# Performance work log

Hardware: AMD Instinct MI355X
Metric: run time of the kernel (lower is better)

Reference implementation:

```python
import jax, jax.numpy as jnp
import numpy as np

NEG_BIG = -9e15
ALPHA = 0.2  # LeakyReLU negative slope


def setup_inputs() -> dict:
    key = jax.random.key(0)
    k1, k2, k3, k4 = jax.random.split(key, 4)
    B, N, IN, OUT = 8, 2048, 128, 64
    x = jax.random.normal(k1, (B, N, IN), dtype=jnp.float32)
    adj = jax.random.randint(k2, (B, N, N), 0, 2, dtype=jnp.int32)
    # xavier_uniform with gain=1.414
    lim_W = 1.414 * np.sqrt(6.0 / (IN + OUT))
    W = jax.random.uniform(k3, (IN, OUT), jnp.float32, -lim_W, lim_W)
    lim_a = 1.414 * np.sqrt(6.0 / (2 * OUT + 1))
    a = jax.random.uniform(k4, (2 * OUT, 1), jnp.float32, -lim_a, lim_a)
    return {"x": x, "adj": adj, "W": W, "a": a}


def reference(x, adj, W, a):
    # h: [B, N, out_dim]
    h = jnp.matmul(x, W)
    out_dim = W.shape[1]
    a1 = a[:out_dim, 0]   # applied to h_i (row / destination)
    a2 = a[out_dim:, 0]   # applied to h_j (col / source)
    # e_ij = leakyrelu(h_i . a1 + h_j . a2)  -- avoids the O(B*N*N*2d) concat
    si = jnp.einsum('bnd,d->bn', h, a1)  # [B, N]
    sj = jnp.einsum('bnd,d->bn', h, a2)  # [B, N]
    e = si[:, :, None] + sj[:, None, :]  # [B, N, N]
    e = jnp.where(e > 0, e, ALPHA * e)   # LeakyReLU
    e = jnp.where(adj > 0, e, NEG_BIG)
    attention = jax.nn.softmax(e, axis=-1)  # [B, N, N]
    # dropout p=0.0 (eval mode): identity
    h_prime = jnp.matmul(attention, h)       # [B, N, out_dim]
    return h_prime, attention
```

## Files before the change

### kernel.cpp

```cpp
#include <hip/hip_runtime.h>

#define BB 8
#define NN 2048
#define IND 128
#define OUTD 64
#define ALPHA 0.2f

typedef __attribute__((ext_vector_type(8))) short bf16x8;
typedef __attribute__((ext_vector_type(4))) float f32x4;
typedef unsigned int u32;

__global__ __launch_bounds__(256) void k1_hproj(const float* __restrict__ x,
                                                const float* __restrict__ W,
                                                const float* __restrict__ a,
                                                short* __restrict__ hT_hi,
                                                short* __restrict__ hT_lo,
                                                float* __restrict__ si,
                                                float* __restrict__ sj) {
    __shared__ float Wl[IND * OUTD];
    __shared__ float xl[16][IND];
    __shared__ float tile[16][OUTD + 1];
    int t = threadIdx.x, lane = t & 63, wave = t >> 6;

    const float4* W4 = (const float4*)W;
    float4* Wl4 = (float4*)Wl;
    #pragma unroll
    for (int q = 0; q < 8; ++q) Wl4[t + q * 256] = W4[t + q * 256];

    int row0 = blockIdx.x * 16;
    const float4* x4 = (const float4*)(x + (size_t)row0 * IND);
    float4* xl4 = (float4*)&xl[0][0];
    xl4[t] = x4[t];
    xl4[t + 256] = x4[t + 256];
    __syncthreads();

    float a1v = a[lane];
    float a2v = a[OUTD + lane];

    float acc[4] = {0.f, 0.f, 0.f, 0.f};
    int rbase = wave * 4;
    for (int k = 0; k < IND; k += 4) {
        float4 xv0 = *(const float4*)&xl[rbase + 0][k];
        float4 xv1 = *(const float4*)&xl[rbase + 1][k];
        float4 xv2 = *(const float4*)&xl[rbase + 2][k];
        float4 xv3 = *(const float4*)&xl[rbase + 3][k];
        #pragma unroll
        for (int q = 0; q < 4; ++q) {
            float w = Wl[(k + q) * OUTD + lane];
            acc[0] = fmaf(((const float*)&xv0)[q], w, acc[0]);
            acc[1] = fmaf(((const float*)&xv1)[q], w, acc[1]);
            acc[2] = fmaf(((const float*)&xv2)[q], w, acc[2]);
            acc[3] = fmaf(((const float*)&xv3)[q], w, acc[3]);
        }
    }
    #pragma unroll
    for (int rr = 0; rr < 4; ++rr) {
        size_t grow = (size_t)row0 + rbase + rr;
        tile[rbase + rr][lane] = acc[rr];
        float v1 = acc[rr] * a1v;
        float v2 = acc[rr] * a2v;
        #pragma unroll
        for (int o = 32; o; o >>= 1) {
            v1 += __shfl_xor(v1, o);
            v2 += __shfl_xor(v2, o);
        }
        if (lane == 0) { si[grow] = v1; sj[grow] = v2; }
    }
    __syncthreads();

    int d = t >> 2, kq = (t & 3) * 4;
    int b = row0 >> 11;
    int krow = (row0 & (NN - 1)) + kq;
    float v0 = tile[kq + 0][d], v1 = tile[kq + 1][d];
    float v2 = tile[kq + 2][d], v3 = tile[kq + 3][d];
    u32 b0 = __float_as_uint(v0), b1 = __float_as_uint(v1);
    u32 b2 = __float_as_uint(v2), b3 = __float_as_uint(v3);
    u32 h0 = b0 & 0xffff0000u, h1 = b1 & 0xffff0000u;
    u32 h2 = b2 & 0xffff0000u, h3 = b3 & 0xffff0000u;
    float l0 = v0 - __uint_as_float(h0), l1 = v1 - __uint_as_float(h1);
    float l2 = v2 - __uint_as_float(h2), l3 = v3 - __uint_as_float(h3);
    uint2 hi2, lo2;
    hi2.x = (b0 >> 16) | h1;
    hi2.y = (b2 >> 16) | h3;
    lo2.x = (__float_as_uint(l0) >> 16) | (__float_as_uint(l1) & 0xffff0000u);
    lo2.y = (__float_as_uint(l2) >> 16) | (__float_as_uint(l3) & 0xffff0000u);
    size_t off = ((size_t)b * OUTD + d) * NN + krow;
    *(uint2*)(hT_hi + off) = hi2;
    *(uint2*)(hT_lo + off) = lo2;
}

__global__ __launch_bounds__(512) void k23(const int* __restrict__ adj,
                                           const float* __restrict__ si,
                                           const float* __restrict__ sj,
                                           const short* __restrict__ hT_hi,
                                           const short* __restrict__ hT_lo,
                                           float* __restrict__ attn,
                                           float* __restrict__ hp) {
    __shared__ unsigned char mask_lds[16][264];
    __shared__ float si_lds[16], inv_lds[16];
    __shared__ f32x4 red[8][4][64];

    int t = threadIdx.x, lane = t & 63, w = t >> 6;
    int bk = blockIdx.x;
    int b = bk >> 7;
    int i0 = (bk & 127) * 16;
    size_t rowbase = (size_t)b * NN + i0;
    const float* sjb = sj + (size_t)b * NN;
    const f32x4* sjb4 = (const f32x4*)sjb;

    #pragma unroll
    for (int rr = 0; rr < 2; ++rr) {
        int row = w * 2 + rr;
        size_t grow = rowbase + row;
        float s_i = si[grow];
        const int4* arow = (const int4*)(adj + grow * NN);
        float sum = 0.f;
        #pragma unroll
        for (int q = 0; q < 8; ++q) {
            int4 av = arow[q * 64 + lane];
            f32x4 sv = sjb4[q * 64 + lane];
            unsigned nib = 0;
            float e, pe;
            e = s_i + sv.x; e = e > 0.f ? e : ALPHA * e; pe = __expf(e);
            if (av.x > 0) { nib |= 1u; sum += pe; }
            e = s_i + sv.y; e = e > 0.f ? e : ALPHA * e; pe = __expf(e);
            if (av.y > 0) { nib |= 2u; sum += pe; }
            e = s_i + sv.z; e = e > 0.f ? e : ALPHA * e; pe = __expf(e);
            if (av.z > 0) { nib |= 4u; sum += pe; }
            e = s_i + sv.w; e = e > 0.f ? e : ALPHA * e; pe = __expf(e);
            if (av.w > 0) { nib |= 8u; sum += pe; }
            unsigned pn = (unsigned)__shfl_xor((int)nib, 1);
            if (!(lane & 1))
                mask_lds[row][q * 32 + (lane >> 1)] = (unsigned char)(nib | (pn << 4));
        }
        #pragma unroll
        for (int o = 32; o; o >>= 1) sum += __shfl_xor(sum, o);
        if (lane == 0) {
            si_lds[row] = s_i;
            inv_lds[row] = sum > 0.f ? 1.0f / sum : 0.f;
        }
    }
    __syncthreads();

    {
        f32x4 sv = sjb4[t];
        int mbyte = t >> 1;
        int nshift = (t & 1) * 4;
        #pragma unroll 4
        for (int row = 0; row < 16; ++row) {
            unsigned nib = ((unsigned)mask_lds[row][mbyte] >> nshift) & 0xFu;
            float s_i = si_lds[row], inv = inv_lds[row];
            f32x4 pv;
            float e;
            e = s_i + sv.x; e = e > 0.f ? e : ALPHA * e;
            pv.x = (nib & 1u) ? __expf(e) * inv : 0.f;
            e = s_i + sv.y; e = e > 0.f ? e : ALPHA * e;
            pv.y = (nib & 2u) ? __expf(e) * inv : 0.f;
            e = s_i + sv.z; e = e > 0.f ? e : ALPHA * e;
            pv.z = (nib & 4u) ? __expf(e) * inv : 0.f;
            e = s_i + sv.w; e = e > 0.f ? e : ALPHA * e;
            pv.w = (nib & 8u) ? __expf(e) * inv : 0.f;
            __builtin_nontemporal_store(pv,
                (f32x4*)(attn + (rowbase + row) * (size_t)NN + (size_t)t * 4));
        }
    }

    int m = lane & 15, g = lane >> 4;
    float si_m = si_lds[m];
    float inv_m = inv_lds[m];
    const short* bh_base = hT_hi + ((size_t)b * OUTD + m) * NN;
    const short* bl_base = hT_lo + ((size_t)b * OUTD + m) * NN;

    f32x4 acc[4];
    #pragma unroll
    for (int tt = 0; tt < 4; ++tt) acc[tt] = (f32x4){0.f, 0.f, 0.f, 0.f};

    for (int step = 0; step < 8; ++step) {
        int jb = w * 256 + step * 32 + g * 8;
        f32x4 s0 = *(const f32x4*)(sjb + jb);
        f32x4 s1 = *(const f32x4*)(sjb + jb + 4);
        unsigned mb = mask_lds[m][jb >> 3];
        float sv[8] = {s0.x, s0.y, s0.z, s0.w, s1.x, s1.y, s1.z, s1.w};
        float p[8];
        #pragma unroll
        for (int q = 0; q < 8; ++q) {
            float e = si_m + sv[q];
            e = e > 0.f ? e : ALPHA * e;
            float pe = __expf(e) * inv_m;
            p[q] = ((mb >> q) & 1u) ? pe : 0.f;
        }

        union { bf16x8 v; u32 u[4]; } ph, pl;
        #pragma unroll
        for (int q = 0; q < 4; ++q) {
            u32 c0 = __float_as_uint(p[2 * q]), c1 = __float_as_uint(p[2 * q + 1]);
            u32 t0 = c0 & 0xffff0000u, t1 = c1 & 0xffff0000u;
            float d0 = p[2 * q] - __uint_as_float(t0);
            float d1 = p[2 * q + 1] - __uint_as_float(t1);
            ph.u[q] = (c0 >> 16) | t1;
            pl.u[q] = (__float_as_uint(d0) >> 16) | (__float_as_uint(d1) & 0xffff0000u);
        }

        #pragma unroll
        for (int tt = 0; tt < 4; ++tt) {
            bf16x8 bh = *(const bf16x8*)(bh_base + (size_t)tt * 16 * NN + jb);
            bf16x8 bl = *(const bf16x8*)(bl_base + (size_t)tt * 16 * NN + jb);
            acc[tt] = __builtin_amdgcn_mfma_f32_16x16x32_bf16(ph.v, bh, acc[tt], 0, 0, 0);
            acc[tt] = __builtin_amdgcn_mfma_f32_16x16x32_bf16(ph.v, bl, acc[tt], 0, 0, 0);
            acc[tt] = __builtin_amdgcn_mfma_f32_16x16x32_bf16(pl.v, bh, acc[tt], 0, 0, 0);
        }
    }

    #pragma unroll
    for (int tt = 0; tt < 4; ++tt) red[w][tt][lane] = acc[tt];
    __syncthreads();

    #pragma unroll
    for (int idx = t; idx < 16 * OUTD; idx += 512) {
        int row = idx >> 6, n = idx & 63;
        int ln = (row >> 2) * 16 + (n & 15);
        int reg = row & 3;
        float v = 0.f;
        #pragma unroll
        for (int ww = 0; ww < 8; ++ww)
            v += ((const float*)&red[ww][n >> 4][ln])[reg];
        hp[(rowbase + row) * OUTD + n] = v;
    }
}

extern "C" void kernel_launch(void* const* d_in, const int* in_sizes, int n_in,
                              void* d_out, int out_size, void* d_ws, size_t ws_size,
                              hipStream_t stream) {
    const float* x   = (const float*)d_in[0];
    const int*   adj = (const int*)d_in[1];
    const float* W   = (const float*)d_in[2];
    const float* a   = (const float*)d_in[3];

    float* out  = (float*)d_out;
    float* hp   = out;
    float* attn = out + (size_t)BB * NN * OUTD;

    char* ws = (char*)d_ws;
    short* hT_hi = (short*)ws;
    short* hT_lo = hT_hi + (size_t)BB * OUTD * NN;
    float* si    = (float*)(hT_lo + (size_t)BB * OUTD * NN);
    float* sj    = si + (size_t)BB * NN;

    k1_hproj<<<BB * NN / 16, 256, 0, stream>>>(x, W, a, hT_hi, hT_lo, si, sj);
    k23<<<BB * NN / 16, 512, 0, stream>>>(adj, si, sj, hT_hi, hT_lo, attn, hp);
}
```

Before: 124.9 us.

## Persistent two-tile blocks with register-prefetched adjacency and fused attn/P staging

The k23 kernel becomes persistent: 512 blocks each process two 16-row tiles, and the adjacency rows for the second tile are prefetched into registers while the first tile computes. The separate attention-write pass and the per-wave MFMA probability recompute are merged into one chunked loop. Each wave computes its rows' probabilities once, stores them to attn, and writes bf16 hi/lo splits to LDS, where all waves read them for the MFMA. The goal is to hide adjacency load latency and avoid computing the exponentials twice. In exchange it adds two LDS barriers per chunk, uses heavy register pressure (areg holds 64 VGPRs), and relies on a hand-written lgkmcnt-only barrier.

```diff
diff --git a/kernel.cpp b/kernel.cpp
--- a/kernel.cpp
+++ b/kernel.cpp
@@ -5,10 +5,15 @@
 #define IND 128
 #define OUTD 64
 #define ALPHA 0.2f
+#define NBLK 512
 
 typedef __attribute__((ext_vector_type(8))) short bf16x8;
 typedef __attribute__((ext_vector_type(4))) float f32x4;
 typedef unsigned int u32;
+
+__device__ __forceinline__ void bar_lds() {
+    asm volatile("s_waitcnt lgkmcnt(0)\n\ts_barrier" ::: "memory");
+}
 
 __global__ __launch_bounds__(256) void k1_hproj(const float* __restrict__ x,
                                                 const float* __restrict__ W,
@@ -89,142 +94,158 @@
     *(uint2*)(hT_lo + off) = lo2;
 }
 
-__global__ __launch_bounds__(512) void k23(const int* __restrict__ adj,
-                                           const float* __restrict__ si,
-                                           const float* __restrict__ sj,
-                                           const short* __restrict__ hT_hi,
-                                           const short* __restrict__ hT_lo,
-                                           float* __restrict__ attn,
-                                           float* __restrict__ hp) {
-    __shared__ unsigned char mask_lds[16][264];
-    __shared__ float si_lds[16], inv_lds[16];
+__global__ __launch_bounds__(512, 2) void k23(const int* __restrict__ adj,
+                                              const float* __restrict__ si,
+                                              const float* __restrict__ sj,
+                                              const short* __restrict__ hT_hi,
+                                              const short* __restrict__ hT_lo,
+                                              float* __restrict__ attn,
+                                              float* __restrict__ hp) {
+    __shared__ short p_hi[16][264];
+    __shared__ short p_lo[16][264];
     __shared__ f32x4 red[8][4][64];
 
     int t = threadIdx.x, lane = t & 63, w = t >> 6;
     int bk = blockIdx.x;
-    int b = bk >> 7;
-    int i0 = (bk & 127) * 16;
-    size_t rowbase = (size_t)b * NN + i0;
-    const float* sjb = sj + (size_t)b * NN;
-    const f32x4* sjb4 = (const f32x4*)sjb;
-
-    #pragma unroll
-    for (int rr = 0; rr < 2; ++rr) {
-        int row = w * 2 + rr;
-        size_t grow = rowbase + row;
-        float s_i = si[grow];
-        const int4* arow = (const int4*)(adj + grow * NN);
-        float sum = 0.f;
+    int r0 = w * 2;
+    int m = lane & 15, g = lane >> 4;
+
+    int4 areg[2][8];
+
+    {
+        size_t grow = (size_t)(bk >> 7) * NN + (size_t)(bk & 127) * 16 + r0;
+        const int4* a0 = (const int4*)(adj + grow * NN);
+        const int4* a1 = (const int4*)(adj + (grow + 1) * NN);
         #pragma unroll
         for (int q = 0; q < 8; ++q) {
-            int4 av = arow[q * 64 + lane];
-            f32x4 sv = sjb4[q * 64 + lane];
-            unsigned nib = 0;
-            float e, pe;
-            e = s_i + sv.x; e = e > 0.f ? e : ALPHA * e; pe = __expf(e);
-            if (av.x > 0) { nib |= 1u; sum += pe; }
-            e = s_i + sv.y; e = e > 0.f ? e : ALPHA * e; pe = __expf(e);
-            if (av.y > 0) { nib |= 2u; sum += pe; }
-            e = s_i + sv.z; e = e > 0.f ? e : ALPHA * e; pe = __expf(e);
-            if (av.z > 0) { nib |= 4u; sum += pe; }
-            e = s_i + sv.w; e = e > 0.f ? e : ALPHA * e; pe = __expf(e);
-            if (av.w > 0) { nib |= 8u; sum += pe; }
-            unsigned pn = (unsigned)__shfl_xor((int)nib, 1);
-            if (!(lane & 1))
-                mask_lds[row][q * 32 + (lane >> 1)] = (unsigned char)(nib | (pn << 4));
-        }
-        #pragma unroll
-        for (int o = 32; o; o >>= 1) sum += __shfl_xor(sum, o);
-        if (lane == 0) {
-            si_lds[row] = s_i;
-            inv_lds[row] = sum > 0.f ? 1.0f / sum : 0.f;
-        }
-    }
-    __syncthreads();
-
-    {
-        f32x4 sv = sjb4[t];
-        int mbyte = t >> 1;
-        int nshift = (t & 1) * 4;
-        #pragma unroll 4
-        for (int row = 0; row < 16; ++row) {
-            unsigned nib = ((unsigned)mask_lds[row][mbyte] >> nshift) & 0xFu;
-            float s_i = si_lds[row], inv = inv_lds[row];
-            f32x4 pv;
-            float e;
-            e = s_i + sv.x; e = e > 0.f ? e : ALPHA * e;
-            pv.x = (nib & 1u) ? __expf(e) * inv : 0.f;
-            e = s_i + sv.y; e = e > 0.f ? e : ALPHA * e;
-            pv.y = (nib & 2u) ? __expf(e) * inv : 0.f;
-            e = s_i + sv.z; e = e > 0.f ? e : ALPHA * e;
-            pv.z = (nib & 4u) ? __expf(e) * inv : 0.f;
-            e = s_i + sv.w; e = e > 0.f ? e : ALPHA * e;
-            pv.w = (nib & 8u) ? __expf(e) * inv : 0.f;
-            __builtin_nontemporal_store(pv,
-                (f32x4*)(attn + (rowbase + row) * (size_t)NN + (size_t)t * 4));
-        }
-    }
-
-    int m = lane & 15, g = lane >> 4;
-    float si_m = si_lds[m];
-    float inv_m = inv_lds[m];
-    const short* bh_base = hT_hi + ((size_t)b * OUTD + m) * NN;
-    const short* bl_base = hT_lo + ((size_t)b * OUTD + m) * NN;
-
-    f32x4 acc[4];
-    #pragma unroll
-    for (int tt = 0; tt < 4; ++tt) acc[tt] = (f32x4){0.f, 0.f, 0.f, 0.f};
-
-    for (int step = 0; step < 8; ++step) {
-        int jb = w * 256 + step * 32 + g * 8;
-        f32x4 s0 = *(const f32x4*)(sjb + jb);
-        f32x4 s1 = *(const f32x4*)(sjb + jb + 4);
-        unsigned mb = mask_lds[m][jb >> 3];
-        float sv[8] = {s0.x, s0.y, s0.z, s0.w, s1.x, s1.y, s1.z, s1.w};
-        float p[8];
-        #pragma unroll
-        for (int q = 0; q < 8; ++q) {
-            float e = si_m + sv[q];
-            e = e > 0.f ? e : ALPHA * e;
-            float pe = __expf(e) * inv_m;
-            p[q] = ((mb >> q) & 1u) ? pe : 0.f;
-        }
-
-        union { bf16x8 v; u32 u[4]; } ph, pl;
-        #pragma unroll
-        for (int q = 0; q < 4; ++q) {
-            u32 c0 = __float_as_uint(p[2 * q]), c1 = __float_as_uint(p[2 * q + 1]);
-            u32 t0 = c0 & 0xffff0000u, t1 = c1 & 0xffff0000u;
-            float d0 = p[2 * q] - __uint_as_float(t0);
-            float d1 = p[2 * q + 1] - __uint_as_float(t1);
-            ph.u[q] = (c0 >> 16) | t1;
-            pl.u[q] = (__float_as_uint(d0) >> 16) | (__float_as_uint(d1) & 0xffff0000u);
-        }
-
-        #pragma unroll
-        for (int tt = 0; tt < 4; ++tt) {
-            bf16x8 bh = *(const bf16x8*)(bh_base + (size_t)tt * 16 * NN + jb);
-            bf16x8 bl = *(const bf16x8*)(bl_base + (size_t)tt * 16 * NN + jb);
-            acc[tt] = __builtin_amdgcn_mfma_f32_16x16x32_bf16(ph.v, bh, acc[tt], 0, 0, 0);
-            acc[tt] = __builtin_amdgcn_mfma_f32_16x16x32_bf16(ph.v, bl, acc[tt], 0, 0, 0);
-            acc[tt] = __builtin_amdgcn_mfma_f32_16x16x32_bf16(pl.v, bh, acc[tt], 0, 0, 0);
-        }
-    }
-
-    #pragma unroll
-    for (int tt = 0; tt < 4; ++tt) red[w][tt][lane] = acc[tt];
-    __syncthreads();
-
-    #pragma unroll
-    for (int idx = t; idx < 16 * OUTD; idx += 512) {
-        int row = idx >> 6, n = idx & 63;
-        int ln = (row >> 2) * 16 + (n & 15);
-        int reg = row & 3;
-        float v = 0.f;
-        #pragma unroll
-        for (int ww = 0; ww < 8; ++ww)
-            v += ((const float*)&red[ww][n >> 4][ln])[reg];
-        hp[(rowbase + row) * OUTD + n] = v;
+            areg[0][q] = a0[q * 64 + lane];
+            areg[1][q] = a1[q * 64 + lane];
+        }
+    }
+
+    for (int it = 0; it < 2; ++it) {
+        int T = bk + it * NBLK;
+        int b = T >> 7;
+        int i0 = (T & 127) * 16;
+        size_t rowbase = (size_t)b * NN + i0;
+        const float* sjb = sj + (size_t)b * NN;
+        const f32x4* sjb4 = (const f32x4*)sjb;
+
+        u32 mask32[2];
+        float inv[2], siv[2];
+        #pragma unroll
+        for (int r = 0; r < 2; ++r) {
+            float s_i = si[rowbase + r0 + r];
+            siv[r] = s_i;
+            float sum = 0.f;
+            u32 mk = 0;
+            #pragma unroll
+            for (int q = 0; q < 8; ++q) {
+                f32x4 sv = sjb4[q * 64 + lane];
+                int4 av = areg[r][q];
+                float e, pe;
+                e = s_i + sv.x; e = e > 0.f ? e : ALPHA * e; pe = __expf(e);
+                if (av.x > 0) { mk |= 1u << (q * 4 + 0); sum += pe; }
+                e = s_i + sv.y; e = e > 0.f ? e : ALPHA * e; pe = __expf(e);
+                if (av.y > 0) { mk |= 1u << (q * 4 + 1); sum += pe; }
+                e = s_i + sv.z; e = e > 0.f ? e : ALPHA * e; pe = __expf(e);
+                if (av.z > 0) { mk |= 1u << (q * 4 + 2); sum += pe; }
+                e = s_i + sv.w; e = e > 0.f ? e : ALPHA * e; pe = __expf(e);
+                if (av.w > 0) { mk |= 1u << (q * 4 + 3); sum += pe; }
+            }
+            #pragma unroll
+            for (int o = 32; o; o >>= 1) sum += __shfl_xor(sum, o);
+            mask32[r] = mk;
+            inv[r] = sum > 0.f ? 1.0f / sum : 0.f;
+        }
+
+        if (it == 0) {
+            int T2 = bk + NBLK;
+            size_t grow2 = (size_t)(T2 >> 7) * NN + (size_t)(T2 & 127) * 16 + r0;
+            const int4* a0 = (const int4*)(adj + grow2 * NN);
+            const int4* a1 = (const int4*)(adj + (grow2 + 1) * NN);
+            #pragma unroll
+            for (int q = 0; q < 8; ++q) {
+                areg[0][q] = a0[q * 64 + lane];
+                areg[1][q] = a1[q * 64 + lane];
+            }
+        }
+
+        f32x4 acc[4];
+        #pragma unroll
+        for (int tt = 0; tt < 4; ++tt) acc[tt] = (f32x4){0.f, 0.f, 0.f, 0.f};
+
+        const short* bh0 = hT_hi + ((size_t)b * OUTD + m) * NN;
+        const short* bl0 = hT_lo + ((size_t)b * OUTD + m) * NN;
+
+        for (int c = 0; c < 8; ++c) {
+            f32x4 sv = sjb4[c * 64 + lane];
+            #pragma unroll
+            for (int r = 0; r < 2; ++r) {
+                int row = r0 + r;
+                u32 nib = (mask32[r] >> (c * 4)) & 0xFu;
+                float s_i = siv[r], iv = inv[r];
+                float e, p0, p1, p2, p3;
+                e = s_i + sv.x; e = e > 0.f ? e : ALPHA * e;
+                p0 = (nib & 1u) ? __expf(e) * iv : 0.f;
+                e = s_i + sv.y; e = e > 0.f ? e : ALPHA * e;
+                p1 = (nib & 2u) ? __expf(e) * iv : 0.f;
+                e = s_i + sv.z; e = e > 0.f ? e : ALPHA * e;
+                p2 = (nib & 4u) ? __expf(e) * iv : 0.f;
+                e = s_i + sv.w; e = e > 0.f ? e : ALPHA * e;
+                p3 = (nib & 8u) ? __expf(e) * iv : 0.f;
+
+                f32x4 pv = {p0, p1, p2, p3};
+                __builtin_nontemporal_store(pv,
+                    (f32x4*)(attn + (rowbase + row) * (size_t)NN + c * 256 + lane * 4));
+
+                u32 c0 = __float_as_uint(p0), c1 = __float_as_uint(p1);
+                u32 c2 = __float_as_uint(p2), c3 = __float_as_uint(p3);
+                u32 h0 = c0 & 0xffff0000u, h1 = c1 & 0xffff0000u;
+                u32 h2 = c2 & 0xffff0000u, h3 = c3 & 0xffff0000u;
+                float d0 = p0 - __uint_as_float(h0), d1 = p1 - __uint_as_float(h1);
+                float d2 = p2 - __uint_as_float(h2), d3 = p3 - __uint_as_float(h3);
+                uint2 hiw, low;
+                hiw.x = (c0 >> 16) | h1;
+                hiw.y = (c2 >> 16) | h3;
+                low.x = (__float_as_uint(d0) >> 16) | (__float_as_uint(d1) & 0xffff0000u);
+                low.y = (__float_as_uint(d2) >> 16) | (__float_as_uint(d3) & 0xffff0000u);
+                *(uint2*)&p_hi[row][lane * 4] = hiw;
+                *(uint2*)&p_lo[row][lane * 4] = low;
+            }
+            bar_lds();
+
+            int kl = w * 32 + g * 8;
+            int kk = c * 256 + kl;
+            bf16x8 ph = *(const bf16x8*)&p_hi[m][kl];
+            bf16x8 pl = *(const bf16x8*)&p_lo[m][kl];
+            #pragma unroll
+            for (int tt = 0; tt < 4; ++tt) {
+                bf16x8 bh = *(const bf16x8*)(bh0 + (size_t)tt * 16 * NN + kk);
+                bf16x8 bl = *(const bf16x8*)(bl0 + (size_t)tt * 16 * NN + kk);
+                acc[tt] = __builtin_amdgcn_mfma_f32_16x16x32_bf16(ph, bh, acc[tt], 0, 0, 0);
+                acc[tt] = __builtin_amdgcn_mfma_f32_16x16x32_bf16(ph, bl, acc[tt], 0, 0, 0);
+                acc[tt] = __builtin_amdgcn_mfma_f32_16x16x32_bf16(pl, bh, acc[tt], 0, 0, 0);
+            }
+            bar_lds();
+        }
+
+        #pragma unroll
+        for (int tt = 0; tt < 4; ++tt) red[w][tt][lane] = acc[tt];
+        bar_lds();
+
+        #pragma unroll
+        for (int idx = t; idx < 16 * OUTD; idx += 512) {
+            int row = idx >> 6, n = idx & 63;
+            int ln = (row >> 2) * 16 + (n & 15);
+            int reg = row & 3;
+            float v = 0.f;
+            #pragma unroll
+            for (int ww = 0; ww < 8; ++ww)
+                v += ((const float*)&red[ww][n >> 4][ln])[reg];
+            hp[(rowbase + row) * OUTD + n] = v;
+        }
+        bar_lds();
     }
 }
 
@@ -247,5 +268,5 @@
     float* sj    = si + (size_t)BB * NN;
 
     k1_hproj<<<BB * NN / 16, 256, 0, stream>>>(x, W, a, hT_hi, hT_lo, si, sj);
-    k23<<<BB * NN / 16, 512, 0, stream>>>(adj, si, sj, hT_hi, hT_lo, attn, hp);
-}
+    k23<<<NBLK, 512, 0, stream>>>(adj, si, sj, hT_hi, hT_lo, attn, hp);
+}
```

Result: slower. 156.8 us (+25.5%).
